# Kernel tuning notes

Measured on AMD Instinct MI355X. Metric: run time of the kernel, lower is better.

Reference implementation:

```python
import jax, jax.numpy as jnp
import numpy as np
import math

HEAD_N = 8
IN_FEATS = 512
BATCH, LENG = 4, 2048
LN_EPS = 1e-5


def setup_inputs() -> dict:
    key = jax.random.key(0)
    ks = jax.random.split(key, 16)
    d = IN_FEATS
    inp = {
        "q": jax.random.normal(ks[0], (BATCH, LENG, d), jnp.float32),
        "k": jax.random.normal(ks[1], (BATCH, LENG, d), jnp.float32),
        "v": jax.random.normal(ks[2], (BATCH, LENG, d), jnp.float32),
        # 4 Linear(in_feats, in_feats): weights [out,in] torch-style, bias [out]
        "Wq": jax.random.normal(ks[3], (d, d), jnp.float32) * 0.02,
        "bq": jnp.zeros((d,), jnp.float32),
        "Wk": jax.random.normal(ks[4], (d, d), jnp.float32) * 0.02,
        "bk": jnp.zeros((d,), jnp.float32),
        "Wv": jax.random.normal(ks[5], (d, d), jnp.float32) * 0.02,
        "bv": jnp.zeros((d,), jnp.float32),
        "Wo": jax.random.normal(ks[6], (d, d), jnp.float32) * 0.02,
        "bo": jnp.zeros((d,), jnp.float32),
        "gamma": jnp.ones((d,), jnp.float32),
        "beta": jnp.zeros((d,), jnp.float32),
    }
    return inp


def _split_heads(x, W, b):
    # Linear then reshape exactly as the torch code: (B,L,D)->(B,L,H,dh)->(B,H,L,dh)->(B*H,L,dh)
    B, L, D = x.shape
    dh = D // HEAD_N
    y = x @ W.T + b
    y = y.reshape(B, L, HEAD_N, dh).transpose(0, 2, 1, 3).reshape(B * HEAD_N, L, dh)
    return y


def reference(q, k, v, Wq, bq, Wk, bk, Wv, bv, Wo, bo, gamma, beta):
    residual = q
    B, L, D = q.shape
    dh = D // HEAD_N
    qh = _split_heads(q, Wq, bq)  # [B*H, L, dh]
    kh = _split_heads(k, Wk, bk)
    vh = _split_heads(v, Wv, bv)

    scores = jnp.einsum("nqd,nkd->nqk", qh, kh) / math.sqrt(dh)  # [B*H, L, L]
    raw_att = jax.nn.softmax(scores, axis=-1)
    att = jnp.einsum("nqk,nkd->nqd", raw_att, vh)  # [B*H, L, dh]

    # Faithful to the original (buggy) merge: reshape (B*H,L,dh) AS IF layout were (H,B,L,dh)
    att = att.reshape(HEAD_N, B, L, dh).transpose(1, 2, 0, 3).reshape(B, L, D)

    att = att @ Wo.T + bo
    # dropout is identity in eval/reference mode
    x = att + residual
    mu = jnp.mean(x, axis=-1, keepdims=True)
    var = jnp.mean(jnp.square(x - mu), axis=-1, keepdims=True)
    out = (x - mu) / jnp.sqrt(var + LN_EPS) * gamma + beta
    return (out, raw_att)
```

## Files before the change

### kernel.cpp

```cpp
#include <hip/hip_runtime.h>
#include <hip/hip_bf16.h>

#define D_MODEL 512
#define SEQ 2048
#define NB 4
#define NH 8
#define DH 64
#define NHEADS 32
#define MROWS 8192

typedef __bf16 bf16_t;
typedef __bf16 bf16x4_t __attribute__((ext_vector_type(4)));
typedef __bf16 bf16x8_t __attribute__((ext_vector_type(8)));
typedef float f32x4_t __attribute__((ext_vector_type(4)));

__device__ inline f32x4_t mfma16(bf16x8_t a, bf16x8_t b, f32x4_t c) {
    return __builtin_amdgcn_mfma_f32_16x16x32_bf16(a, b, c, 0, 0, 0);
}

template<int MODE>
__global__ __launch_bounds__(256) void qkv_proj_kernel(
    const float* __restrict__ X, const float* __restrict__ W,
    const float* __restrict__ bias, bf16_t* __restrict__ dst)
{
    __shared__ bf16_t As[128][72];
    __shared__ bf16_t Bs[128][72];

    const int t = threadIdx.x;
    const int lane = t & 63, w = t >> 6;
    const int lr = lane & 15, lg = lane >> 4;
    const int wm = w >> 1, wn = w & 1;
    const int m0 = blockIdx.x * 128, n0 = blockIdx.y * 128;

    f32x4_t acc[4][4];
#pragma unroll
    for (int i = 0; i < 4; i++)
#pragma unroll
        for (int j = 0; j < 4; j++) acc[i][j] = f32x4_t{0.f, 0.f, 0.f, 0.f};

    const int srow = t >> 4;
    const int scol = (t & 15) * 4;

    for (int kt = 0; kt < 8; kt++) {
        __syncthreads();
#pragma unroll
        for (int p = 0; p < 8; p++) {
            int row = p * 16 + srow;
            float4 va = *(const float4*)(X + (size_t)(m0 + row) * 512 + kt * 64 + scol);
            bf16x4_t ha = { (bf16_t)va.x, (bf16_t)va.y, (bf16_t)va.z, (bf16_t)va.w };
            *(bf16x4_t*)(&As[row][scol]) = ha;
            float4 vb = *(const float4*)(W + (size_t)(n0 + row) * 512 + kt * 64 + scol);
            bf16x4_t hb = { (bf16_t)vb.x, (bf16_t)vb.y, (bf16_t)vb.z, (bf16_t)vb.w };
            *(bf16x4_t*)(&Bs[row][scol]) = hb;
        }
        __syncthreads();
#pragma unroll
        for (int kk = 0; kk < 64; kk += 32) {
            bf16x8_t fa[4], fb[4];
#pragma unroll
            for (int i = 0; i < 4; i++)
                fa[i] = (MODE == 2)
                    ? *(const bf16x8_t*)(&As[wm * 64 + i * 16 + lr][kk + lg * 8])
                    : *(const bf16x8_t*)(&Bs[wm * 64 + i * 16 + lr][kk + lg * 8]);
#pragma unroll
            for (int j = 0; j < 4; j++)
                fb[j] = (MODE == 2)
                    ? *(const bf16x8_t*)(&Bs[wn * 64 + j * 16 + lr][kk + lg * 8])
                    : *(const bf16x8_t*)(&As[wn * 64 + j * 16 + lr][kk + lg * 8]);
#pragma unroll
            for (int i = 0; i < 4; i++)
#pragma unroll
                for (int j = 0; j < 4; j++)
                    acc[i][j] = mfma16(fa[i], fb[j], acc[i][j]);
        }
    }

    if (MODE == 2) {
#pragma unroll
        for (int j = 0; j < 4; j++) {
            int col = n0 + wn * 64 + j * 16 + lr;
            float bval = bias[col];
            int h = col >> 6, d = col & 63;
#pragma unroll
            for (int i = 0; i < 4; i++) {
                int rbase = m0 + wm * 64 + i * 16 + lg * 4;
                int b = rbase >> 11, l0 = rbase & 2047;
                int win = l0 >> 5, kkg = l0 & 31;
                int pos0 = (kkg < 16) ? ((kkg >> 2) * 8) : (((kkg - 16) >> 2) * 8 + 4);
                bf16x4_t hv;
#pragma unroll
                for (int r = 0; r < 4; r++) hv[r] = (bf16_t)(acc[i][j][r] + bval);
                *(bf16x4_t*)(dst + ((((size_t)(b * NH + h) * 64 + win) * 64 + d) * 32 + pos0)) = hv;
            }
        }
    } else {
#pragma unroll
        for (int i = 0; i < 4; i++) {
            int featbase = n0 + wm * 64 + i * 16 + lg * 4;
            float4 b4 = *(const float4*)(bias + featbase);
            float bb[4] = { b4.x, b4.y, b4.z, b4.w };
            int h = featbase >> 6, d0 = featbase & 63;
            int c = (d0 & 31) >> 3, e0 = d0 & 7, fd = (d0 >= 32) ? 1 : 0;
#pragma unroll
            for (int j = 0; j < 4; j++) {
                int seq = m0 + wn * 64 + j * 16 + lr;
                int b = seq >> 11, l = seq & 2047;
                bf16x4_t hv;
#pragma unroll
                for (int r = 0; r < 4; r++) hv[r] = (bf16_t)(acc[i][j][r] + bb[r]);
                size_t idx;
                if (MODE == 0) {
                    int qw = l >> 4, lp = (l & 15) + 16 * c;
                    idx = ((((size_t)(b * NH + h) * 128 + qw) * 2 + fd) * 64 + lp) * 8 + e0;
                } else {
                    int win = l >> 5, fk = (((l & 31) >= 16) ? 2 : 0) + fd;
                    int lp = (l & 15) + 16 * c;
                    idx = ((((size_t)(b * NH + h) * 64 + win) * 4 + fk) * 64 + lp) * 8 + e0;
                }
                *(bf16x4_t*)(dst + idx) = hv;
            }
        }
    }
}

__global__ __launch_bounds__(256, 4) void attn_kernel(
    const bf16_t* __restrict__ qfrag, const bf16_t* __restrict__ kfrag,
    const bf16_t* __restrict__ vfrag, float* __restrict__ probs,
    bf16_t* __restrict__ attw)
{
    __shared__ float stage[4][16][132];

    const int bh = blockIdx.y;
    const int t = threadIdx.x;
    const int lane = t & 63, w = t >> 6;
    const int lr = lane & 15, lg = lane >> 4;
    const int q0 = blockIdx.x * 64 + w * 16;
    const int qw = q0 >> 4;

    const bf16_t* qfb = qfrag + (size_t)bh * 131072;
    const bf16x8_t qf0 = *(const bf16x8_t*)(qfb + ((size_t)(qw * 2 + 0) * 64 + lane) * 8);
    const bf16x8_t qf1 = *(const bf16x8_t*)(qfb + ((size_t)(qw * 2 + 1) * 64 + lane) * 8);

    const bf16_t* kfb = kfrag + (size_t)bh * 131072;
    const bf16_t* vfb = vfrag + (size_t)bh * 64 * 64 * 32;
    float* pb = probs + (size_t)bh * SEQ * SEQ + (size_t)q0 * SEQ;

    float sum = 0.f;
    {
        const bf16_t* kp0 = kfb + lane * 8;
        bf16x8_t k00 = *(const bf16x8_t*)(kp0);
        bf16x8_t k01 = *(const bf16x8_t*)(kp0 + 512);
        bf16x8_t k10 = *(const bf16x8_t*)(kp0 + 1024);
        bf16x8_t k11 = *(const bf16x8_t*)(kp0 + 1536);
#pragma unroll 2
        for (int win = 0; win < 64; win++) {
            bf16x8_t n00 = k00, n01 = k01, n10 = k10, n11 = k11;
            if (win < 63) {
                const bf16_t* kp = kfb + (size_t)(win + 1) * 2048 + lane * 8;
                n00 = *(const bf16x8_t*)(kp);
                n01 = *(const bf16x8_t*)(kp + 512);
                n10 = *(const bf16x8_t*)(kp + 1024);
                n11 = *(const bf16x8_t*)(kp + 1536);
            }
            f32x4_t s0 = {0.f, 0.f, 0.f, 0.f}, s1 = {0.f, 0.f, 0.f, 0.f};
            s0 = mfma16(k00, qf0, s0);
            s0 = mfma16(k01, qf1, s0);
            s1 = mfma16(k10, qf0, s1);
            s1 = mfma16(k11, qf1, s1);
#pragma unroll
            for (int r = 0; r < 4; r++)
                sum += __expf(s0[r] * 0.125f) + __expf(s1[r] * 0.125f);
            k00 = n00; k01 = n01; k10 = n10; k11 = n11;
        }
    }
    sum += __shfl_xor(sum, 16, 64);
    sum += __shfl_xor(sum, 32, 64);
    const float ri = 1.0f / sum;

    f32x4_t oacc[4];
#pragma unroll
    for (int db = 0; db < 4; db++) oacc[db] = f32x4_t{0.f, 0.f, 0.f, 0.f};

    {
        const bf16_t* kp0 = kfb + lane * 8;
        bf16x8_t k00 = *(const bf16x8_t*)(kp0);
        bf16x8_t k01 = *(const bf16x8_t*)(kp0 + 512);
        bf16x8_t k10 = *(const bf16x8_t*)(kp0 + 1024);
        bf16x8_t k11 = *(const bf16x8_t*)(kp0 + 1536);

        for (int sw = 0; sw < 16; sw++) {
#pragma unroll
            for (int c = 0; c < 4; c++) {
                const int win = sw * 4 + c;
                bf16x8_t av[4];
#pragma unroll
                for (int db = 0; db < 4; db++)
                    av[db] = *(const bf16x8_t*)(vfb + (((size_t)win * 64 + db * 16 + lr) * 32 + lg * 8));
                bf16x8_t n00 = k00, n01 = k01, n10 = k10, n11 = k11;
                if (win < 63) {
                    const bf16_t* kp = kfb + (size_t)(win + 1) * 2048 + lane * 8;
                    n00 = *(const bf16x8_t*)(kp);
                    n01 = *(const bf16x8_t*)(kp + 512);
                    n10 = *(const bf16x8_t*)(kp + 1024);
                    n11 = *(const bf16x8_t*)(kp + 1536);
                }
                f32x4_t s0 = {0.f, 0.f, 0.f, 0.f}, s1 = {0.f, 0.f, 0.f, 0.f};
                s0 = mfma16(k00, qf0, s0);
                s0 = mfma16(k01, qf1, s0);
                s1 = mfma16(k10, qf0, s1);
                s1 = mfma16(k11, qf1, s1);
                float pl[8];
#pragma unroll
                for (int r = 0; r < 4; r++) {
                    pl[r]     = __expf(s0[r] * 0.125f) * ri;
                    pl[4 + r] = __expf(s1[r] * 0.125f) * ri;
                }
                const int c0 = c * 32;
                f32x4_t lo = { pl[0], pl[1], pl[2], pl[3] };
                f32x4_t hi = { pl[4], pl[5], pl[6], pl[7] };
                *(f32x4_t*)(&stage[w][lr][c0 + lg * 4])      = lo;
                *(f32x4_t*)(&stage[w][lr][c0 + 16 + lg * 4]) = hi;
                bf16x8_t p;
#pragma unroll
                for (int e = 0; e < 8; e++) p[e] = (bf16_t)pl[e];
#pragma unroll
                for (int db = 0; db < 4; db++)
                    oacc[db] = mfma16(av[db], p, oacc[db]);
                k00 = n00; k01 = n01; k10 = n10; k11 = n11;
            }
#pragma unroll
            for (int it = 0; it < 8; it++) {
                int row = it * 2 + (lane >> 5);
                int col = (lane & 31) * 4;
                f32x4_t vv = *(const f32x4_t*)(&stage[w][row][col]);
                __builtin_nontemporal_store(vv, (f32x4_t*)(pb + (size_t)row * SEQ + sw * 128 + col));
            }
        }
    }

    float* ow = &stage[w][0][0];
#pragma unroll
    for (int db = 0; db < 4; db++)
#pragma unroll
        for (int r = 0; r < 4; r++)
            ow[(db * 16 + lg * 4 + r) * 17 + lr] = oacc[db][r];

    bf16x8_t h0, h1;
#pragma unroll
    for (int jj = 0; jj < 8; jj++) h0[jj] = (bf16_t)ow[(lg * 16 + jj) * 17 + lr];
#pragma unroll
    for (int jj = 0; jj < 8; jj++) h1[jj] = (bf16_t)ow[(lg * 16 + 8 + jj) * 17 + lr];
    bf16_t* ao = attw + ((size_t)bh * SEQ + q0 + lr) * DH + lg * 16;
    *(bf16x8_t*)(ao)     = h0;
    *(bf16x8_t*)(ao + 8) = h1;
}

__global__ __launch_bounds__(256) void out_proj_kernel(
    const bf16_t* __restrict__ attw, const float* __restrict__ Wo,
    const float* __restrict__ bo, float* __restrict__ y)
{
    __shared__ bf16_t As[128][72];
    __shared__ bf16_t Bs[128][72];

    const int t = threadIdx.x;
    const int lane = t & 63, w = t >> 6;
    const int lr = lane & 15, lg = lane >> 4;
    const int wm = w >> 1, wn = w & 1;
    const int m0 = blockIdx.x * 128, n0 = blockIdx.y * 128;

    f32x4_t acc[4][4];
#pragma unroll
    for (int i = 0; i < 4; i++)
#pragma unroll
        for (int j = 0; j < 4; j++) acc[i][j] = f32x4_t{0.f, 0.f, 0.f, 0.f};

    const int arow = t >> 3;
    const int acol = (t & 7) * 8;
    const int srow = t >> 4;
    const int scol = (t & 15) * 4;

    for (int kt = 0; kt < 8; kt++) {
        __syncthreads();
#pragma unroll
        for (int p = 0; p < 4; p++) {
            int row = p * 32 + arow;
            int grow = m0 + row;
            int b = grow >> 11, l = grow & 2047;
            bf16x8_t va = *(const bf16x8_t*)(attw + (size_t)((kt * NB + b) * SEQ + l) * DH + acol);
            *(bf16x8_t*)(&As[row][acol]) = va;
        }
#pragma unroll
        for (int p = 0; p < 8; p++) {
            int row = p * 16 + srow;
            float4 vb = *(const float4*)(Wo + (size_t)(n0 + row) * 512 + kt * 64 + scol);
            bf16x4_t hb = { (bf16_t)vb.x, (bf16_t)vb.y, (bf16_t)vb.z, (bf16_t)vb.w };
            *(bf16x4_t*)(&Bs[row][scol]) = hb;
        }
        __syncthreads();
#pragma unroll
        for (int kk = 0; kk < 64; kk += 32) {
            bf16x8_t af[4], bfr[4];
#pragma unroll
            for (int i = 0; i < 4; i++)
                af[i] = *(const bf16x8_t*)(&As[wm * 64 + i * 16 + lr][kk + lg * 8]);
#pragma unroll
            for (int j = 0; j < 4; j++)
                bfr[j] = *(const bf16x8_t*)(&Bs[wn * 64 + j * 16 + lr][kk + lg * 8]);
#pragma unroll
            for (int i = 0; i < 4; i++)
#pragma unroll
                for (int j = 0; j < 4; j++)
                    acc[i][j] = mfma16(af[i], bfr[j], acc[i][j]);
        }
    }

#pragma unroll
    for (int j = 0; j < 4; j++) {
        int col = n0 + wn * 64 + j * 16 + lr;
        float bval = bo[col];
#pragma unroll
        for (int i = 0; i < 4; i++) {
#pragma unroll
            for (int r = 0; r < 4; r++) {
                int row = m0 + wm * 64 + i * 16 + lg * 4 + r;
                y[(size_t)row * 512 + col] = acc[i][j][r] + bval;
            }
        }
    }
}

__global__ __launch_bounds__(256) void ln_kernel(
    const float* __restrict__ y, const float* __restrict__ resid,
    const float* __restrict__ gamma, const float* __restrict__ beta,
    float* __restrict__ out)
{
    const int t = threadIdx.x;
    const int lane = t & 63, w = t >> 6;
    const int row = blockIdx.x * 4 + w;
    const float* yr = y + (size_t)row * 512;
    const float* rr = resid + (size_t)row * 512;
    const int c = lane * 8;

    float4 a0 = *(const float4*)(yr + c);
    float4 a1 = *(const float4*)(yr + c + 4);
    float4 r0 = *(const float4*)(rr + c);
    float4 r1 = *(const float4*)(rr + c + 4);
    float x[8] = { a0.x + r0.x, a0.y + r0.y, a0.z + r0.z, a0.w + r0.w,
                   a1.x + r1.x, a1.y + r1.y, a1.z + r1.z, a1.w + r1.w };

    float s = 0.f, sq = 0.f;
#pragma unroll
    for (int e = 0; e < 8; e++) { s += x[e]; sq += x[e] * x[e]; }
#pragma unroll
    for (int msk = 32; msk >= 1; msk >>= 1) {
        s  += __shfl_xor(s,  msk, 64);
        sq += __shfl_xor(sq, msk, 64);
    }
    float mean = s * (1.f / 512.f);
    float var  = sq * (1.f / 512.f) - mean * mean;
    float rstd = rsqrtf(var + 1e-5f);

    float4 g0 = *(const float4*)(gamma + c);
    float4 g1 = *(const float4*)(gamma + c + 4);
    float4 b0 = *(const float4*)(beta + c);
    float4 b1 = *(const float4*)(beta + c + 4);
    float g[8] = { g0.x, g0.y, g0.z, g0.w, g1.x, g1.y, g1.z, g1.w };
    float bb[8] = { b0.x, b0.y, b0.z, b0.w, b1.x, b1.y, b1.z, b1.w };

    float o[8];
#pragma unroll
    for (int e = 0; e < 8; e++) o[e] = (x[e] - mean) * rstd * g[e] + bb[e];
    float4 o0 = { o[0], o[1], o[2], o[3] };
    float4 o1 = { o[4], o[5], o[6], o[7] };
    float* op = out + (size_t)row * 512 + c;
    *(float4*)(op)     = o0;
    *(float4*)(op + 4) = o1;
}

extern "C" void kernel_launch(void* const* d_in, const int* in_sizes, int n_in,
                              void* d_out, int out_size, void* d_ws, size_t ws_size,
                              hipStream_t stream)
{
    (void)in_sizes; (void)n_in; (void)out_size; (void)ws_size;

    const float* q     = (const float*)d_in[0];
    const float* k     = (const float*)d_in[1];
    const float* v     = (const float*)d_in[2];
    const float* Wq    = (const float*)d_in[3];
    const float* bq    = (const float*)d_in[4];
    const float* Wk    = (const float*)d_in[5];
    const float* bk    = (const float*)d_in[6];
    const float* Wv    = (const float*)d_in[7];
    const float* bv    = (const float*)d_in[8];
    const float* Wo    = (const float*)d_in[9];
    const float* bo    = (const float*)d_in[10];
    const float* gamma = (const float*)d_in[11];
    const float* beta  = (const float*)d_in[12];

    float* out   = (float*)d_out;
    float* probs = out + (size_t)NB * SEQ * D_MODEL;

    char* ws = (char*)d_ws;
    bf16_t* qfrag = (bf16_t*)(ws);
    bf16_t* kfrag = (bf16_t*)(ws + 8388608);
    bf16_t* vfrag = (bf16_t*)(ws + 16777216);
    bf16_t* attw  = (bf16_t*)(ws + 25165824);
    float*  y     = (float*) (ws + 33554432);

    qkv_proj_kernel<0><<<dim3(64, 4), 256, 0, stream>>>(q, Wq, bq, qfrag);
    qkv_proj_kernel<1><<<dim3(64, 4), 256, 0, stream>>>(k, Wk, bk, kfrag);
    qkv_proj_kernel<2><<<dim3(64, 4), 256, 0, stream>>>(v, Wv, bv, vfrag);
    attn_kernel<<<dim3(32, 32), 256, 0, stream>>>(qfrag, kfrag, vfrag, probs, attw);
    out_proj_kernel<<<dim3(64, 4), 256, 0, stream>>>(attw, Wo, bo, y);
    ln_kernel<<<2048, 256, 0, stream>>>(y, q, gamma, beta, out);
}
```

Measured before the change: 224.3 us.

## Merge QKV projections into one launch and pipeline two query chunks per attention wave

The three QKV projection launches become a single launch with blockIdx.z selecting Q, K or V. Each attention wave now handles two 16-row query chunks. The row-sum pass for the second chunk is folded into the probability/PV pass of the first, which removes a separate K sweep for half the rows. Each block covers 128 query rows, occupancy is lowered to 2 blocks per SM, and the grid is halved. The trade-off is more register pressure and less parallelism in exchange for fewer K passes.

```diff
diff --git a/kernel.cpp b/kernel.cpp
--- a/kernel.cpp
+++ b/kernel.cpp
@@ -18,13 +18,21 @@
     return __builtin_amdgcn_mfma_f32_16x16x32_bf16(a, b, c, 0, 0, 0);
 }
 
-template<int MODE>
-__global__ __launch_bounds__(256) void qkv_proj_kernel(
-    const float* __restrict__ X, const float* __restrict__ W,
-    const float* __restrict__ bias, bf16_t* __restrict__ dst)
+__global__ __launch_bounds__(256) void qkv_proj_all_kernel(
+    const float* __restrict__ qp, const float* __restrict__ kp, const float* __restrict__ vp,
+    const float* __restrict__ Wq, const float* __restrict__ bq,
+    const float* __restrict__ Wk, const float* __restrict__ bk,
+    const float* __restrict__ Wv, const float* __restrict__ bv,
+    bf16_t* __restrict__ qfrag, bf16_t* __restrict__ kfrag, bf16_t* __restrict__ vfrag)
 {
     __shared__ bf16_t As[128][72];
     __shared__ bf16_t Bs[128][72];
+
+    const int mode = blockIdx.z;
+    const float* X    = (mode == 0) ? qp : (mode == 1) ? kp : vp;
+    const float* W    = (mode == 0) ? Wq : (mode == 1) ? Wk : Wv;
+    const float* bias = (mode == 0) ? bq : (mode == 1) ? bk : bv;
+    bf16_t* dst       = (mode == 0) ? qfrag : (mode == 1) ? kfrag : vfrag;
 
     const int t = threadIdx.x;
     const int lane = t & 63, w = t >> 6;
@@ -40,6 +48,9 @@
 
     const int srow = t >> 4;
     const int scol = (t & 15) * 4;
+
+    bf16_t (*Pa)[72] = (mode == 2) ? As : Bs;
+    bf16_t (*Pb)[72] = (mode == 2) ? Bs : As;
 
     for (int kt = 0; kt < 8; kt++) {
         __syncthreads();
@@ -59,14 +70,10 @@
             bf16x8_t fa[4], fb[4];
 #pragma unroll
             for (int i = 0; i < 4; i++)
-                fa[i] = (MODE == 2)
-                    ? *(const bf16x8_t*)(&As[wm * 64 + i * 16 + lr][kk + lg * 8])
-                    : *(const bf16x8_t*)(&Bs[wm * 64 + i * 16 + lr][kk + lg * 8]);
+                fa[i] = *(const bf16x8_t*)(&Pa[wm * 64 + i * 16 + lr][kk + lg * 8]);
 #pragma unroll
             for (int j = 0; j < 4; j++)
-                fb[j] = (MODE == 2)
-                    ? *(const bf16x8_t*)(&Bs[wn * 64 + j * 16 + lr][kk + lg * 8])
-                    : *(const bf16x8_t*)(&As[wn * 64 + j * 16 + lr][kk + lg * 8]);
+                fb[j] = *(const bf16x8_t*)(&Pb[wn * 64 + j * 16 + lr][kk + lg * 8]);
 #pragma unroll
             for (int i = 0; i < 4; i++)
 #pragma unroll
@@ -75,7 +82,7 @@
         }
     }
 
-    if (MODE == 2) {
+    if (mode == 2) {
 #pragma unroll
         for (int j = 0; j < 4; j++) {
             int col = n0 + wn * 64 + j * 16 + lr;
@@ -109,7 +116,7 @@
 #pragma unroll
                 for (int r = 0; r < 4; r++) hv[r] = (bf16_t)(acc[i][j][r] + bb[r]);
                 size_t idx;
-                if (MODE == 0) {
+                if (mode == 0) {
                     int qw = l >> 4, lp = (l & 15) + 16 * c;
                     idx = ((((size_t)(b * NH + h) * 128 + qw) * 2 + fd) * 64 + lp) * 8 + e0;
                 } else {
@@ -123,7 +130,7 @@
     }
 }
 
-__global__ __launch_bounds__(256, 4) void attn_kernel(
+__global__ __launch_bounds__(256, 2) void attn_kernel(
     const bf16_t* __restrict__ qfrag, const bf16_t* __restrict__ kfrag,
     const bf16_t* __restrict__ vfrag, float* __restrict__ probs,
     bf16_t* __restrict__ attw)
@@ -134,18 +141,20 @@
     const int t = threadIdx.x;
     const int lane = t & 63, w = t >> 6;
     const int lr = lane & 15, lg = lane >> 4;
-    const int q0 = blockIdx.x * 64 + w * 16;
-    const int qw = q0 >> 4;
+    const int q0c0 = blockIdx.x * 128 + w * 32;
+    const int q0c1 = q0c0 + 16;
+    const int qw0 = q0c0 >> 4;
 
     const bf16_t* qfb = qfrag + (size_t)bh * 131072;
-    const bf16x8_t qf0 = *(const bf16x8_t*)(qfb + ((size_t)(qw * 2 + 0) * 64 + lane) * 8);
-    const bf16x8_t qf1 = *(const bf16x8_t*)(qfb + ((size_t)(qw * 2 + 1) * 64 + lane) * 8);
+    const bf16x8_t qA0 = *(const bf16x8_t*)(qfb + ((size_t)(qw0 * 2 + 0) * 64 + lane) * 8);
+    const bf16x8_t qA1 = *(const bf16x8_t*)(qfb + ((size_t)(qw0 * 2 + 1) * 64 + lane) * 8);
+    const bf16x8_t qB0 = *(const bf16x8_t*)(qfb + ((size_t)(qw0 * 2 + 2) * 64 + lane) * 8);
+    const bf16x8_t qB1 = *(const bf16x8_t*)(qfb + ((size_t)(qw0 * 2 + 3) * 64 + lane) * 8);
 
     const bf16_t* kfb = kfrag + (size_t)bh * 131072;
-    const bf16_t* vfb = vfrag + (size_t)bh * 64 * 64 * 32;
-    float* pb = probs + (size_t)bh * SEQ * SEQ + (size_t)q0 * SEQ;
-
-    float sum = 0.f;
+    const bf16_t* vfb = vfrag + (size_t)bh * 131072;
+
+    float sum0 = 0.f;
     {
         const bf16_t* kp0 = kfb + lane * 8;
         bf16x8_t k00 = *(const bf16x8_t*)(kp0);
@@ -163,25 +172,26 @@
                 n11 = *(const bf16x8_t*)(kp + 1536);
             }
             f32x4_t s0 = {0.f, 0.f, 0.f, 0.f}, s1 = {0.f, 0.f, 0.f, 0.f};
-            s0 = mfma16(k00, qf0, s0);
-            s0 = mfma16(k01, qf1, s0);
-            s1 = mfma16(k10, qf0, s1);
-            s1 = mfma16(k11, qf1, s1);
+            s0 = mfma16(k00, qA0, s0);
+            s0 = mfma16(k01, qA1, s0);
+            s1 = mfma16(k10, qA0, s1);
+            s1 = mfma16(k11, qA1, s1);
 #pragma unroll
             for (int r = 0; r < 4; r++)
-                sum += __expf(s0[r] * 0.125f) + __expf(s1[r] * 0.125f);
+                sum0 += __expf(s0[r] * 0.125f) + __expf(s1[r] * 0.125f);
             k00 = n00; k01 = n01; k10 = n10; k11 = n11;
         }
     }
-    sum += __shfl_xor(sum, 16, 64);
-    sum += __shfl_xor(sum, 32, 64);
-    const float ri = 1.0f / sum;
+    sum0 += __shfl_xor(sum0, 16, 64);
+    sum0 += __shfl_xor(sum0, 32, 64);
+    const float ri0 = 1.0f / sum0;
 
     f32x4_t oacc[4];
 #pragma unroll
     for (int db = 0; db < 4; db++) oacc[db] = f32x4_t{0.f, 0.f, 0.f, 0.f};
-
+    float sum1 = 0.f;
     {
+        float* pb = probs + (size_t)bh * SEQ * SEQ + (size_t)q0c0 * SEQ;
         const bf16_t* kp0 = kfb + lane * 8;
         bf16x8_t k00 = *(const bf16x8_t*)(kp0);
         bf16x8_t k01 = *(const bf16x8_t*)(kp0 + 512);
@@ -205,27 +215,35 @@
                     n11 = *(const bf16x8_t*)(kp + 1536);
                 }
                 f32x4_t s0 = {0.f, 0.f, 0.f, 0.f}, s1 = {0.f, 0.f, 0.f, 0.f};
-                s0 = mfma16(k00, qf0, s0);
-                s0 = mfma16(k01, qf1, s0);
-                s1 = mfma16(k10, qf0, s1);
-                s1 = mfma16(k11, qf1, s1);
+                s0 = mfma16(k00, qA0, s0);
+                s0 = mfma16(k01, qA1, s0);
+                s1 = mfma16(k10, qA0, s1);
+                s1 = mfma16(k11, qA1, s1);
                 float pl[8];
 #pragma unroll
                 for (int r = 0; r < 4; r++) {
-                    pl[r]     = __expf(s0[r] * 0.125f) * ri;
-                    pl[4 + r] = __expf(s1[r] * 0.125f) * ri;
+                    pl[r]     = __expf(s0[r] * 0.125f) * ri0;
+                    pl[4 + r] = __expf(s1[r] * 0.125f) * ri0;
                 }
-                const int c0 = c * 32;
+                const int c0_ = c * 32;
                 f32x4_t lo = { pl[0], pl[1], pl[2], pl[3] };
                 f32x4_t hi = { pl[4], pl[5], pl[6], pl[7] };
-                *(f32x4_t*)(&stage[w][lr][c0 + lg * 4])      = lo;
-                *(f32x4_t*)(&stage[w][lr][c0 + 16 + lg * 4]) = hi;
+                *(f32x4_t*)(&stage[w][lr][c0_ + lg * 4])      = lo;
+                *(f32x4_t*)(&stage[w][lr][c0_ + 16 + lg * 4]) = hi;
                 bf16x8_t p;
 #pragma unroll
                 for (int e = 0; e < 8; e++) p[e] = (bf16_t)pl[e];
 #pragma unroll
                 for (int db = 0; db < 4; db++)
                     oacc[db] = mfma16(av[db], p, oacc[db]);
+                f32x4_t u0 = {0.f, 0.f, 0.f, 0.f}, u1 = {0.f, 0.f, 0.f, 0.f};
+                u0 = mfma16(k00, qB0, u0);
+                u0 = mfma16(k01, qB1, u0);
+                u1 = mfma16(k10, qB0, u1);
+                u1 = mfma16(k11, qB1, u1);
+#pragma unroll
+                for (int r = 0; r < 4; r++)
+                    sum1 += __expf(u0[r] * 0.125f) + __expf(u1[r] * 0.125f);
                 k00 = n00; k01 = n01; k10 = n10; k11 = n11;
             }
 #pragma unroll
@@ -237,22 +255,103 @@
             }
         }
     }
-
-    float* ow = &stage[w][0][0];
-#pragma unroll
-    for (int db = 0; db < 4; db++)
-#pragma unroll
-        for (int r = 0; r < 4; r++)
-            ow[(db * 16 + lg * 4 + r) * 17 + lr] = oacc[db][r];
-
-    bf16x8_t h0, h1;
-#pragma unroll
-    for (int jj = 0; jj < 8; jj++) h0[jj] = (bf16_t)ow[(lg * 16 + jj) * 17 + lr];
-#pragma unroll
-    for (int jj = 0; jj < 8; jj++) h1[jj] = (bf16_t)ow[(lg * 16 + 8 + jj) * 17 + lr];
-    bf16_t* ao = attw + ((size_t)bh * SEQ + q0 + lr) * DH + lg * 16;
-    *(bf16x8_t*)(ao)     = h0;
-    *(bf16x8_t*)(ao + 8) = h1;
+    sum1 += __shfl_xor(sum1, 16, 64);
+    sum1 += __shfl_xor(sum1, 32, 64);
+    const float ri1 = 1.0f / sum1;
+
+    {
+        float* ow = &stage[w][0][0];
+#pragma unroll
+        for (int db = 0; db < 4; db++)
+#pragma unroll
+            for (int r = 0; r < 4; r++)
+                ow[(db * 16 + lg * 4 + r) * 17 + lr] = oacc[db][r];
+        bf16x8_t h0, h1;
+#pragma unroll
+        for (int jj = 0; jj < 8; jj++) h0[jj] = (bf16_t)ow[(lg * 16 + jj) * 17 + lr];
+#pragma unroll
+        for (int jj = 0; jj < 8; jj++) h1[jj] = (bf16_t)ow[(lg * 16 + 8 + jj) * 17 + lr];
+        bf16_t* ao = attw + ((size_t)bh * SEQ + q0c0 + lr) * DH + lg * 16;
+        *(bf16x8_t*)(ao)     = h0;
+        *(bf16x8_t*)(ao + 8) = h1;
+    }
+
+#pragma unroll
+    for (int db = 0; db < 4; db++) oacc[db] = f32x4_t{0.f, 0.f, 0.f, 0.f};
+    {
+        float* pb = probs + (size_t)bh * SEQ * SEQ + (size_t)q0c1 * SEQ;
+        const bf16_t* kp0 = kfb + lane * 8;
+        bf16x8_t k00 = *(const bf16x8_t*)(kp0);
+        bf16x8_t k01 = *(const bf16x8_t*)(kp0 + 512);
+        bf16x8_t k10 = *(const bf16x8_t*)(kp0 + 1024);
+        bf16x8_t k11 = *(const bf16x8_t*)(kp0 + 1536);
+
+        for (int sw = 0; sw < 16; sw++) {
+#pragma unroll
+            for (int c = 0; c < 4; c++) {
+                const int win = sw * 4 + c;
+                bf16x8_t av[4];
+#pragma unroll
+                for (int db = 0; db < 4; db++)
+                    av[db] = *(const bf16x8_t*)(vfb + (((size_t)win * 64 + db * 16 + lr) * 32 + lg * 8));
+                bf16x8_t n00 = k00, n01 = k01, n10 = k10, n11 = k11;
+                if (win < 63) {
+                    const bf16_t* kp = kfb + (size_t)(win + 1) * 2048 + lane * 8;
+                    n00 = *(const bf16x8_t*)(kp);
+                    n01 = *(const bf16x8_t*)(kp + 512);
+                    n10 = *(const bf16x8_t*)(kp + 1024);
+                    n11 = *(const bf16x8_t*)(kp + 1536);
+                }
+                f32x4_t s0 = {0.f, 0.f, 0.f, 0.f}, s1 = {0.f, 0.f, 0.f, 0.f};
+                s0 = mfma16(k00, qB0, s0);
+                s0 = mfma16(k01, qB1, s0);
+                s1 = mfma16(k10, qB0, s1);
+                s1 = mfma16(k11, qB1, s1);
+                float pl[8];
+#pragma unroll
+                for (int r = 0; r < 4; r++) {
+                    pl[r]     = __expf(s0[r] * 0.125f) * ri1;
+                    pl[4 + r] = __expf(s1[r] * 0.125f) * ri1;
+                }
+                const int c0_ = c * 32;
+                f32x4_t lo = { pl[0], pl[1], pl[2], pl[3] };
+                f32x4_t hi = { pl[4], pl[5], pl[6], pl[7] };
+                *(f32x4_t*)(&stage[w][lr][c0_ + lg * 4])      = lo;
+                *(f32x4_t*)(&stage[w][lr][c0_ + 16 + lg * 4]) = hi;
+                bf16x8_t p;
+#pragma unroll
+                for (int e = 0; e < 8; e++) p[e] = (bf16_t)pl[e];
+#pragma unroll
+                for (int db = 0; db < 4; db++)
+                    oacc[db] = mfma16(av[db], p, oacc[db]);
+                k00 = n00; k01 = n01; k10 = n10; k11 = n11;
+            }
+#pragma unroll
+            for (int it = 0; it < 8; it++) {
+                int row = it * 2 + (lane >> 5);
+                int col = (lane & 31) * 4;
+                f32x4_t vv = *(const f32x4_t*)(&stage[w][row][col]);
+                __builtin_nontemporal_store(vv, (f32x4_t*)(pb + (size_t)row * SEQ + sw * 128 + col));
+            }
+        }
+    }
+
+    {
+        float* ow = &stage[w][0][0];
+#pragma unroll
+        for (int db = 0; db < 4; db++)
+#pragma unroll
+            for (int r = 0; r < 4; r++)
+                ow[(db * 16 + lg * 4 + r) * 17 + lr] = oacc[db][r];
+        bf16x8_t h0, h1;
+#pragma unroll
+        for (int jj = 0; jj < 8; jj++) h0[jj] = (bf16_t)ow[(lg * 16 + jj) * 17 + lr];
+#pragma unroll
+        for (int jj = 0; jj < 8; jj++) h1[jj] = (bf16_t)ow[(lg * 16 + 8 + jj) * 17 + lr];
+        bf16_t* ao = attw + ((size_t)bh * SEQ + q0c1 + lr) * DH + lg * 16;
+        *(bf16x8_t*)(ao)     = h0;
+        *(bf16x8_t*)(ao + 8) = h1;
+    }
 }
 
 __global__ __launch_bounds__(256) void out_proj_kernel(
@@ -407,10 +506,9 @@
     bf16_t* attw  = (bf16_t*)(ws + 25165824);
     float*  y     = (float*) (ws + 33554432);
 
-    qkv_proj_kernel<0><<<dim3(64, 4), 256, 0, stream>>>(q, Wq, bq, qfrag);
-    qkv_proj_kernel<1><<<dim3(64, 4), 256, 0, stream>>>(k, Wk, bk, kfrag);
-    qkv_proj_kernel<2><<<dim3(64, 4), 256, 0, stream>>>(v, Wv, bv, vfrag);
-    attn_kernel<<<dim3(32, 32), 256, 0, stream>>>(qfrag, kfrag, vfrag, probs, attw);
+    qkv_proj_all_kernel<<<dim3(64, 4, 3), 256, 0, stream>>>(
+        q, k, v, Wq, bq, Wk, bk, Wv, bv, qfrag, kfrag, vfrag);
+    attn_kernel<<<dim3(16, 32), 256, 0, stream>>>(qfrag, kfrag, vfrag, probs, attw);
     out_proj_kernel<<<dim3(64, 4), 256, 0, stream>>>(attw, Wo, bo, y);
     ln_kernel<<<2048, 256, 0, stream>>>(y, q, gamma, beta, out);
 }
```

Measured after the change: 203.8 us. 9.2% less time.
